# Performance work log

Measured on AMD Instinct MI355X. Metric: run time of the kernel, lower is better.

The kernel has to match this reference:

```python
import jax, jax.numpy as jnp
import numpy as np

EPS = 1e-5

def inorm(x):
    # instance norm over time (last) axis; torch.std is unbiased (ddof=1)
    m = jnp.mean(x, axis=-1, keepdims=True)
    s = jnp.sqrt(jnp.var(x, axis=-1, ddof=1, keepdims=True))
    return (x - m) / (s + EPS)

def tinorm(x):
    # time-wise instance norm: normalize over channel axis (dim=1)
    m = jnp.mean(x, axis=1, keepdims=True)
    s = jnp.sqrt(jnp.var(x, axis=1, ddof=1, keepdims=True))
    return (x - m) / (s + EPS)

def adaptive_norm(src, trg, wq, wk, wv, norm_fn):
    # src, trg: [B,C,T]; wq/wk/wv: [out,in] as in nn.Linear
    temp = src.shape[1] ** 0.5
    q = jnp.einsum('bct,oc->bto', norm_fn(src), wq)        # [B,Ts,C]
    k = jnp.einsum('bct,oc->bto', norm_fn(trg), wk)        # [B,Tt,C]
    v = jnp.einsum('bct,oc->bto', trg, wv)                 # [B,Tt,C]
    attn = jax.nn.softmax(jnp.einsum('bsc,btc->bst', q / temp, k), axis=-1)
    mean = jnp.einsum('bst,btc->bsc', attn, v)             # attn-weighted mean
    var = jax.nn.relu(jnp.einsum('bst,btc->bsc', attn, v * v) - mean * mean)
    mean_c = jnp.mean(mean, axis=1)[:, :, None]            # [B,C,1]
    std_c = jnp.sqrt(jnp.mean(var, axis=1))[:, :, None]    # [B,C,1]
    return std_c * inorm(src) + mean_c

def sap(x, w, b):
    # self-attention pooling over axis 1; x: [B,N,C], w: [C], b: [1]
    a = jax.nn.softmax(jnp.einsum('bnc,c->bn', x, w) + b, axis=-1)
    return jnp.einsum('bnc,bn->bc', x, a)

def setup_inputs():
    key = jax.random.key(0)
    ks = jax.random.split(key, 24)
    B, C, Ts, Tt, S = 4, 512, 2048, 2048, 2048
    sc = 1.0 / np.sqrt(C).astype(np.float32)
    return {
        'src': jax.random.normal(ks[0], (B, C, Ts), jnp.float32),
        'trg': jax.random.normal(ks[1], (B, C, Tt), jnp.float32),
        'means': jax.random.normal(ks[2], (B, S, C), jnp.float32),
        'stds': jax.random.uniform(ks[3], (B, S, C), jnp.float32),
        'wq_t': jax.random.normal(ks[4], (C, C), jnp.float32) * sc,
        'wk_t': jax.random.normal(ks[5], (C, C), jnp.float32) * sc,
        'wv_t': jax.random.normal(ks[6], (C, C), jnp.float32) * sc,
        'wq_c': jax.random.normal(ks[7], (C, C), jnp.float32) * sc,
        'wk_c': jax.random.normal(ks[8], (C, C), jnp.float32) * sc,
        'wv_c': jax.random.normal(ks[9], (C, C), jnp.float32) * sc,
        'conv1_w': jax.random.normal(ks[10], (C, 2 * C), jnp.float32) * sc,
        'conv1_b': jax.random.normal(ks[11], (C,), jnp.float32) * 0.02,
        'conv2_w': jax.random.normal(ks[12], (C, C, 3), jnp.float32) * sc,
        'bn_g': jax.random.uniform(ks[13], (C,), jnp.float32, 0.5, 1.5),
        'bn_b': jax.random.normal(ks[14], (C,), jnp.float32) * 0.05,
        'bn_m': jax.random.normal(ks[15], (C,), jnp.float32) * 0.1,
        'bn_v': jax.random.uniform(ks[16], (C,), jnp.float32, 0.5, 1.5),
        'msap_w': jax.random.normal(ks[17], (C,), jnp.float32) * sc,
        'msap_b': jax.random.normal(ks[18], (1,), jnp.float32) * 0.02,
        'ssap_w': jax.random.normal(ks[19], (C,), jnp.float32) * sc,
        'ssap_b': jax.random.normal(ks[20], (1,), jnp.float32) * 0.02,
    }

def reference(src, trg, means, stds, wq_t, wk_t, wv_t, wq_c, wk_c, wv_c,
              conv1_w, conv1_b, conv2_w, bn_g, bn_b, bn_m, bn_v,
              msap_w, msap_b, ssap_w, ssap_b):
    src1 = adaptive_norm(src, trg, wq_t, wk_t, wv_t, tinorm)   # TAN
    src2 = adaptive_norm(src, trg, wq_c, wk_c, wv_c, inorm)    # CAN
    x = jnp.concatenate([src1, src2], axis=1)                  # [B,2C,T]
    # conv1: kernel_size=1 -> pointwise GEMM
    x = jnp.einsum('bct,oc->bot', x, conv1_w) + conv1_b[None, :, None]
    # conv2: Conv1d(k=3, pad=1, bias=False) + BatchNorm1d(eval) + ReLU
    x = jax.lax.conv_general_dilated(x, conv2_w, (1,), 'SAME',
                                     dimension_numbers=('NCH', 'OIH', 'NCH'))
    x = (x - bn_m[None, :, None]) * jax.lax.rsqrt(bn_v[None, :, None] + EPS)
    x = x * bn_g[None, :, None] + bn_b[None, :, None]
    x = jax.nn.relu(x)
    # GLAN
    mean = sap(means, msap_w, msap_b)[:, :, None]              # [B,C,1]
    std = sap(stds, ssap_w, ssap_b)[:, :, None]                # [B,C,1]
    return inorm(x) * std + mean
```

## Files before the change

### kernel.cpp

```cpp
#include <hip/hip_runtime.h>
#include <cstdint>
#include <cstddef>

#define B_ 4
#define C_ 512
#define T_ 2048
#define S_ 2048
#define EPSF 1e-5f

typedef __bf16 bf16;
typedef __attribute__((ext_vector_type(8))) __bf16 bf16x8;
typedef __attribute__((ext_vector_type(4))) float f32x4;

__device__ __forceinline__ bf16 f2b(float f){ return (bf16)f; }
__device__ __forceinline__ float b2f(bf16 h){ return (float)h; }

__device__ __forceinline__ void gl_lds16(const void* g, void* l){
  __builtin_amdgcn_global_load_lds((__attribute__((address_space(1))) void*)(g),
                                   (__attribute__((address_space(3))) void*)(l), 16, 0, 0);
}

__device__ __forceinline__ float wave_sum(float v){
#pragma unroll
  for (int o = 32; o; o >>= 1) v += __shfl_xor(v, o, 64);
  return v;
}
__device__ __forceinline__ float wave_max(float v){
#pragma unroll
  for (int o = 32; o; o >>= 1) v = fmaxf(v, __shfl_xor(v, o, 64));
  return v;
}

template<int EPI, int TNW>
__global__ void __launch_bounds__(256) gemm_nt(
    const bf16* __restrict__ A, const bf16* __restrict__ Bm, void* __restrict__ Cout,
    int K, int lda, int ldb, int ldc,
    long long sA, long long sB, long long sC, long long sCb,
    int zdivA, int zmodB, float scale,
    const float* __restrict__ rs, const float* __restrict__ rsh,
    const float* __restrict__ cbias,
    float* __restrict__ osum, float* __restrict__ osum2, long long sRs)
{
  constexpr int TN = TNW*32;
  __shared__ alignas(16) bf16 lA[128*64];
  __shared__ alignas(16) bf16 lB[TN*64];
  const int tid = threadIdx.x;
  const int z = blockIdx.z;
  const bf16* Ab = A + (long long)(z / zdivA) * sA;
  const bf16* Bb = Bm + (long long)(z % zmodB) * sB;
  const int m0 = blockIdx.y*128, n0 = blockIdx.x*TN;
  const int lane = tid & 63, wvi = tid >> 6;
  const int wm = wvi >> 1, wn = wvi & 1;

  f32x4 acc[4][TNW] = {};

  const int lrow = tid >> 3;
  const int lcol = ((tid ^ lrow) & 7) * 8;
  const bf16* pa = Ab + (long long)(m0 + lrow)*lda + lcol;
  const bf16* pb = Bb + (long long)(n0 + lrow)*ldb + lcol;
  char* sa = (char*)lA + tid*16;
  char* sb = (char*)lB + tid*16;

  for (int k0 = 0; k0 < K; k0 += 64) {
#pragma unroll
    for (int it = 0; it < 4; ++it)
      gl_lds16(pa + (long long)it*32*lda + k0, sa + it*4096);
#pragma unroll
    for (int it = 0; it < TNW; ++it)
      gl_lds16(pb + (long long)it*32*ldb + k0, sb + it*4096);
    __syncthreads();
#pragma unroll
    for (int ks = 0; ks < 2; ++ks) {
      const int kq = ks*4 + (lane >> 4);
      bf16x8 af[4], bfr[TNW];
#pragma unroll
      for (int mt = 0; mt < 4; ++mt) {
        int r = wm*64 + mt*16 + (lane & 15);
        af[mt] = *(const bf16x8*)&lA[r*64 + ((kq ^ (r & 7))*8)];
      }
#pragma unroll
      for (int nt = 0; nt < TNW; ++nt) {
        int r = wn*(TNW*16) + nt*16 + (lane & 15);
        bfr[nt] = *(const bf16x8*)&lB[r*64 + ((kq ^ (r & 7))*8)];
      }
#pragma unroll
      for (int mt = 0; mt < 4; ++mt)
#pragma unroll
        for (int nt = 0; nt < TNW; ++nt)
          acc[mt][nt] = __builtin_amdgcn_mfma_f32_16x16x32_bf16(af[mt], bfr[nt], acc[mt][nt], 0, 0, 0);
    }
    __syncthreads();
  }

  if (EPI == 3) {
    float* red1 = (float*)lA;
    float* red2 = red1 + 4*TNW*16;
    const int cr = (lane >> 4)*4;
    float linv[4][4];
#pragma unroll
    for (int mt = 0; mt < 4; ++mt)
#pragma unroll
      for (int i = 0; i < 4; ++i)
        linv[mt][i] = 1.f / rs[(long long)z*sRs + (m0 + wm*64 + mt*16 + cr + i)];
    float s1[TNW], s2[TNW];
#pragma unroll
    for (int nt = 0; nt < TNW; ++nt) {
      s1[nt] = 0.f; s2[nt] = 0.f;
#pragma unroll
      for (int mt = 0; mt < 4; ++mt)
#pragma unroll
        for (int i = 0; i < 4; ++i) {
          float v = acc[mt][nt][i] * linv[mt][i];
          s1[nt] += v; s2[nt] += v*v;
        }
      s1[nt] += __shfl_xor(s1[nt], 16, 64);
      s1[nt] += __shfl_xor(s1[nt], 32, 64);
      s2[nt] += __shfl_xor(s2[nt], 16, 64);
      s2[nt] += __shfl_xor(s2[nt], 32, 64);
    }
    if (lane < 16) {
#pragma unroll
      for (int nt = 0; nt < TNW; ++nt) {
        red1[(wvi*TNW + nt)*16 + lane] = s1[nt];
        red2[(wvi*TNW + nt)*16 + lane] = s2[nt];
      }
    }
    __syncthreads();
    if (tid < 2*TN) {
      const int which = tid >= TN;
      const int col = tid - which*TN;
      const int wn2 = col / (TNW*16), rem = col % (TNW*16);
      const float* rr = which ? red2 : red1;
      float v = rr[wn2*(TNW*16) + rem] + rr[(2+wn2)*(TNW*16) + rem];
      float* dst = which ? osum2 : osum;
      atomicAdd(&dst[sCb*z + n0 + col], v);
    }
    return;
  }

  const int cr = (lane >> 4)*4, cc = lane & 15;
#pragma unroll
  for (int mt = 0; mt < 4; ++mt) {
#pragma unroll
    for (int i = 0; i < 4; ++i) {
      const int mm = m0 + wm*64 + mt*16 + cr + i;
      float rsum = 0.f, rsum2 = 0.f;
#pragma unroll
      for (int nt = 0; nt < TNW; ++nt) {
        const int nn = n0 + wn*(TNW*16) + nt*16 + cc;
        float v = acc[mt][nt][i];
        const long long co = sC*z + (long long)mm*ldc + nn;
        if (EPI == 0) {
          v *= scale;
          if (cbias) v += cbias[sCb*z + nn];
          ((bf16*)Cout)[co] = f2b(v);
        } else if (EPI == 2) {
          v = fmaxf(v*rs[mm] + rsh[mm], 0.f);
          ((float*)Cout)[co] = v;
          rsum += v; rsum2 += v*v;
        } else if (EPI == 4) {
          v = __expf(v);
          ((bf16*)Cout)[co] = f2b(v);
          rsum += v;
        }
      }
      if (EPI == 2 || EPI == 4) {
        rsum += __shfl_xor(rsum, 1, 64); rsum += __shfl_xor(rsum, 2, 64);
        rsum += __shfl_xor(rsum, 4, 64); rsum += __shfl_xor(rsum, 8, 64);
        if (EPI == 2) {
          rsum2 += __shfl_xor(rsum2, 1, 64); rsum2 += __shfl_xor(rsum2, 2, 64);
          rsum2 += __shfl_xor(rsum2, 4, 64); rsum2 += __shfl_xor(rsum2, 8, 64);
        }
        if (cc == 0) {
          atomicAdd(&osum[(long long)z*sRs + mm], rsum);
          if (EPI == 2) atomicAdd(&osum2[(long long)z*sRs + mm], rsum2);
        }
      }
    }
  }
}

__global__ void __launch_bounds__(256) row_stats_k(const float* __restrict__ X1,
    const float* __restrict__ X2, float* __restrict__ Mo, float* __restrict__ So, int n1)
{
  __shared__ float r1[4], r2[4];
  const int row = blockIdx.x;
  const float* x = (row < n1) ? X1 + (long long)row*T_ : X2 + (long long)(row-n1)*T_;
  float s1 = 0.f, s2 = 0.f;
  for (int i = threadIdx.x; i < T_; i += 256){ float v = x[i]; s1 += v; s2 += v*v; }
  s1 = wave_sum(s1); s2 = wave_sum(s2);
  const int lane = threadIdx.x & 63, w = threadIdx.x >> 6;
  if (!lane){ r1[w] = s1; r2[w] = s2; }
  __syncthreads();
  if (threadIdx.x == 0){
    s1 = r1[0]+r1[1]+r1[2]+r1[3];
    s2 = r2[0]+r2[1]+r2[2]+r2[3];
    float m = s1 * (1.f/T_);
    float var = (s2 - s1*m) * (1.f/(T_-1));
    Mo[row] = m; So[row] = sqrtf(fmaxf(var, 0.f));
  }
}

__global__ void __launch_bounds__(256) col_stats_k(const float* __restrict__ src,
    const float* __restrict__ trg, float* __restrict__ Mo, float* __restrict__ So)
{
  __shared__ float r1[4][64], r2[4][64];
  const int z = blockIdx.y, t0 = blockIdx.x*64;
  const float* X = (z < B_) ? src : trg;
  const int b = z & (B_-1);
  const int tl = threadIdx.x & 63, cg = threadIdx.x >> 6;
  float s1 = 0.f, s2 = 0.f;
  for (int c = cg; c < C_; c += 4) {
    float v = X[((long long)b*C_ + c)*T_ + t0 + tl];
    s1 += v; s2 += v*v;
  }
  r1[cg][tl] = s1; r2[cg][tl] = s2;
  __syncthreads();
  if (cg == 0) {
    s1 = r1[0][tl]+r1[1][tl]+r1[2][tl]+r1[3][tl];
    s2 = r2[0][tl]+r2[1][tl]+r2[2][tl]+r2[3][tl];
    float m = s1 * (1.f/C_);
    float var = (s2 - s1*m) * (1.f/(C_-1));
    Mo[z*T_ + t0 + tl] = m;
    So[z*T_ + t0 + tl] = sqrtf(fmaxf(var, 0.f));
  }
}

__global__ void __launch_bounds__(256) transform_k(const float* __restrict__ src,
    const float* __restrict__ trg,
    const float* __restrict__ tnm, const float* __restrict__ tns,
    const float* __restrict__ inm, const float* __restrict__ ins,
    bf16* __restrict__ NSt, bf16* __restrict__ NSc,
    bf16* __restrict__ NTt, bf16* __restrict__ NTc, bf16* __restrict__ TTr)
{
  __shared__ float tile[32][33];
  const int z = blockIdx.z, t0 = blockIdx.x*32, c0 = blockIdx.y*32;
  const int is_t = z >= B_, b = z & (B_-1);
  const float* X = is_t ? trg : src;
  const int tx = threadIdx.x, ty = threadIdx.y;
#pragma unroll
  for (int r = 0; r < 4; ++r) {
    int ci = ty + r*8;
    tile[ci][tx] = X[((long long)b*C_ + c0 + ci)*T_ + t0 + tx];
  }
  __syncthreads();
#pragma unroll
  for (int r = 0; r < 4; ++r) {
    int tj = ty + r*8, ci = tx;
    float v = tile[ci][tj];
    int gt = t0 + tj, gc = c0 + ci;
    float a = (v - tnm[z*T_ + gt]) / (tns[z*T_ + gt] + EPSF);
    float d = (v - inm[z*C_ + gc]) / (ins[z*C_ + gc] + EPSF);
    long long o = ((long long)b*T_ + gt)*C_ + gc;
    if (is_t) { NTt[o] = f2b(a); NTc[o] = f2b(d); TTr[o] = f2b(v); }
    else      { NSt[o] = f2b(a); NSc[o] = f2b(d); }
  }
}

__global__ void __launch_bounds__(256) softmax_row_k(const float* __restrict__ X, float* __restrict__ O)
{
  __shared__ float red[4];
  const long long row = blockIdx.x;
  const float* x = X + row*T_ + threadIdx.x*8;
  float v[8];
  f32x4 a0 = *(const f32x4*)x;
  f32x4 a1 = *(const f32x4*)(x + 4);
#pragma unroll
  for (int j = 0; j < 4; ++j){ v[j] = a0[j]; v[4+j] = a1[j]; }
  float m = -3.4e38f;
#pragma unroll
  for (int j = 0; j < 8; ++j) m = fmaxf(m, v[j]);
  m = wave_max(m);
  const int lane = threadIdx.x & 63, w = threadIdx.x >> 6;
  if (!lane) red[w] = m;
  __syncthreads();
  m = fmaxf(fmaxf(red[0], red[1]), fmaxf(red[2], red[3]));
  __syncthreads();
  float s = 0.f;
#pragma unroll
  for (int j = 0; j < 8; ++j){ v[j] = __expf(v[j] - m); s += v[j]; }
  s = wave_sum(s);
  if (!lane) red[w] = s;
  __syncthreads();
  s = red[0]+red[1]+red[2]+red[3];
  const float inv = 1.f/s;
  float* o = O + row*T_ + threadIdx.x*8;
#pragma unroll
  for (int j = 0; j < 8; ++j) o[j] = v[j]*inv;
}

__global__ void __launch_bounds__(256) colsum_k(const bf16* __restrict__ P,
    const float* __restrict__ l, float* __restrict__ cs)
{
  __shared__ float linv[256];
  const int t = blockIdx.x*256 + threadIdx.x;
  const int z = blockIdx.z;
  const long long s0 = (long long)blockIdx.y*256;
  linv[threadIdx.x] = 1.f / l[(long long)z*S_ + s0 + threadIdx.x];
  __syncthreads();
  const bf16* p = P + ((long long)z*S_ + s0)*T_ + t;
  float a = 0.f;
  for (int s = 0; s < 256; ++s) a += b2f(p[(long long)s*T_]) * linv[s];
  atomicAdd(&cs[z*T_ + t], a);
}

__global__ void __launch_bounds__(256) vv_fin_k(const float* __restrict__ cs,
    const bf16* __restrict__ VT, const float* __restrict__ msum,
    const float* __restrict__ m2sum, float* __restrict__ meanc, float* __restrict__ stdc)
{
  __shared__ float r1[4];
  const int c = blockIdx.x, z = blockIdx.y;
  const bf16* vr = VT + ((long long)z*C_ + c)*T_;
  const float* w = cs + z*T_;
  float a = 0.f;
  for (int t = threadIdx.x; t < T_; t += 256){ float v = b2f(vr[t]); a += w[t]*v*v; }
  a = wave_sum(a);
  const int lane = threadIdx.x & 63, wq = threadIdx.x >> 6;
  if (!lane) r1[wq] = a;
  __syncthreads();
  if (threadIdx.x == 0){
    a = r1[0]+r1[1]+r1[2]+r1[3];
    const int idx = z*C_ + c;
    meanc[idx] = msum[idx] * (1.f/S_);
    float var = (a - m2sum[idx]) * (1.f/S_);
    stdc[idx] = sqrtf(fmaxf(var, 0.f));
  }
}

__global__ void __launch_bounds__(256) weff_k(const float* __restrict__ w1,
    const float* __restrict__ b1, const float* __restrict__ sdt, const float* __restrict__ sdc,
    const float* __restrict__ mct, const float* __restrict__ mcc,
    bf16* __restrict__ Weff, float* __restrict__ beff)
{
  __shared__ float r1[4];
  const int o = blockIdx.x, b = blockIdx.y;
  float accb = 0.f;
  for (int c = threadIdx.x; c < C_; c += 256) {
    float wa = w1[o*2*C_ + c], wb = w1[o*2*C_ + C_ + c];
    Weff[((long long)(b*C_ + o))*C_ + c] = f2b(wa*sdt[b*C_+c] + wb*sdc[b*C_+c]);
    accb += wa*mct[b*C_+c] + wb*mcc[b*C_+c];
  }
  accb = wave_sum(accb);
  const int lane = threadIdx.x & 63, w = threadIdx.x >> 6;
  if (!lane) r1[w] = accb;
  __syncthreads();
  if (threadIdx.x == 0) beff[b*C_ + o] = b1[o] + r1[0]+r1[1]+r1[2]+r1[3];
}

__global__ void __launch_bounds__(256) w2r_k(const float* __restrict__ w2,
    const float* __restrict__ g, const float* __restrict__ be,
    const float* __restrict__ mu, const float* __restrict__ va,
    bf16* __restrict__ W2r, float* __restrict__ bnsc, float* __restrict__ bnsh)
{
  const int o = blockIdx.x;
  for (int c = threadIdx.x; c < C_; c += 256)
#pragma unroll
    for (int dt = 0; dt < 3; ++dt)
      W2r[(long long)o*3*C_ + dt*C_ + c] = f2b(w2[((long long)o*C_ + c)*3 + dt]);
  if (threadIdx.x == 0) {
    float s = g[o] * rsqrtf(va[o] + EPSF);
    bnsc[o] = s;
    bnsh[o] = be[o] - mu[o]*s;
  }
}

__global__ void __launch_bounds__(256) cast6_k(const float* __restrict__ a0,
    const float* __restrict__ a1, const float* __restrict__ a2, const float* __restrict__ a3,
    const float* __restrict__ a4, const float* __restrict__ a5, bf16* __restrict__ o)
{
  const int i = blockIdx.x*256 + threadIdx.x;
  const int slot = i >> 18;
  const float* srcs[6] = {a0,a1,a2,a3,a4,a5};
  const float sc = (slot < 2) ? 0.044194173824159216f : 1.f;
  o[i] = f2b(srcs[slot][i & 262143] * sc);
}

__global__ void __launch_bounds__(256) zero_pad_k(bf16* __restrict__ x1p)
{
  const int i = blockIdx.x*256 + threadIdx.x;
  const int b = i >> 10, rem = i & 1023;
  const long long row = (rem >> 9) ? (T_+1) : 0;
  const int c = rem & (C_-1);
  x1p[((long long)b*(T_+2) + row)*C_ + c] = f2b(0.f);
}

__global__ void __launch_bounds__(256) zero_f32_k(float* __restrict__ p)
{
  p[blockIdx.x*256 + threadIdx.x] = 0.f;
}

__global__ void __launch_bounds__(256) sap_logit_k(const float* __restrict__ means,
    const float* __restrict__ stds, const float* __restrict__ mw, const float* __restrict__ sw,
    const float* __restrict__ mb, const float* __restrict__ sb, float* __restrict__ out)
{
  const int n = blockIdx.x*4 + (threadIdx.x >> 6);
  const int z = blockIdx.y;
  const int sel = z >= B_, b = z & (B_-1);
  const float* x = sel ? stds : means;
  const float* w = sel ? sw : mw;
  const int lane = threadIdx.x & 63;
  const float* p = x + ((long long)b*S_ + n)*C_;
  float a = 0.f;
  for (int c = lane; c < C_; c += 64) a += p[c]*w[c];
  a = wave_sum(a);
  if (!lane) out[z*S_ + n] = a + (sel ? sb[0] : mb[0]);
}

__global__ void __launch_bounds__(256) sap_wsum_k(const float* __restrict__ means,
    const float* __restrict__ stds, const float* __restrict__ a, float* __restrict__ out)
{
  const int c = blockIdx.x*256 + threadIdx.x;
  const int z = blockIdx.z;
  const int sel = z >= B_, b = z & (B_-1);
  const float* x = sel ? stds : means;
  const long long n0 = (long long)blockIdx.y*256;
  const float* p = x + ((long long)b*S_ + n0)*C_ + c;
  const float* aw = a + z*S_ + n0;
  float acc = 0.f;
  for (int n = 0; n < 256; ++n) acc += p[(long long)n*C_] * aw[n];
  atomicAdd(&out[z*C_ + c], acc);
}

__global__ void __launch_bounds__(256) final_k(const float* __restrict__ y,
    const float* __restrict__ ysum, const float* __restrict__ y2sum,
    const float* __restrict__ sapms, float* __restrict__ out)
{
  const long long i = (long long)(blockIdx.x*256 + threadIdx.x) * 4;
  const long long r = i >> 11;
  const float s1 = ysum[r], s2 = y2sum[r];
  const float m = s1 * (1.f/T_);
  const float var = (s2 - s1*m) * (1.f/(T_-1));
  const float inv = 1.f/(sqrtf(fmaxf(var, 0.f)) + EPSF);
  const float mn = sapms[r], sd = sapms[B_*C_ + r];
  const f32x4 v = *(const f32x4*)(y + i);
  f32x4 o;
#pragma unroll
  for (int j = 0; j < 4; ++j) o[j] = (v[j] - m)*inv*sd + mn;
  *(f32x4*)(out + i) = o;
}

extern "C" void kernel_launch(void* const* d_in, const int* in_sizes, int n_in,
                              void* d_out, int out_size, void* d_ws, size_t ws_size,
                              hipStream_t stream)
{
  (void)in_sizes; (void)n_in; (void)out_size; (void)ws_size;
  const float* src    = (const float*)d_in[0];
  const float* trg    = (const float*)d_in[1];
  const float* means  = (const float*)d_in[2];
  const float* stds   = (const float*)d_in[3];
  const float* conv1w = (const float*)d_in[10];
  const float* conv1b = (const float*)d_in[11];
  const float* conv2w = (const float*)d_in[12];
  const float* bn_g   = (const float*)d_in[13];
  const float* bn_b   = (const float*)d_in[14];
  const float* bn_m   = (const float*)d_in[15];
  const float* bn_v   = (const float*)d_in[16];
  const float* msap_w = (const float*)d_in[17];
  const float* msap_b = (const float*)d_in[18];
  const float* ssap_w = (const float*)d_in[19];
  const float* ssap_b = (const float*)d_in[20];

  const long long BTC = (long long)B_*T_*C_;

  char* p = (char*)d_ws;
  auto take = [&](size_t n)->char*{ char* r = p; p += (n + 255) & ~(size_t)255; return r; };

  bf16* NSc = (bf16*)take(BTC*2);
  bf16* P2  = (bf16*)take((size_t)2*B_*S_*T_*2);
  bf16* NSt = P2;
  bf16* NTc = P2 + BTC;
  bf16* NTt = P2 + 2*BTC;
  bf16* TTr = P2 + 3*BTC;
  bf16* QK4 = (bf16*)take((size_t)4*BTC*2);
  bf16* VT2 = (bf16*)take((size_t)2*BTC*2);
  bf16* WQb = (bf16*)take((size_t)6*C_*C_*2);
  bf16* Weff= (bf16*)take((size_t)B_*C_*C_*2);
  bf16* W2r = (bf16*)take((size_t)C_*3*C_*2);
  bf16* x1p = (bf16*)take((size_t)B_*(T_+2)*C_*2);
  float* y  = (float*)take((size_t)B_*C_*T_*4);
  float* colsum = (float*)take(2*B_*T_*4);
  float* msum   = (float*)take(2*B_*C_*4);
  float* m2sum  = (float*)take(2*B_*C_*4);
  float* sapms  = (float*)take(2*B_*C_*4);
  float* lrow   = (float*)take(2*B_*S_*4);
  float* ysum   = (float*)take(B_*C_*4);
  float* y2sum  = (float*)take(B_*C_*4);
  float* tnm = (float*)take(2*B_*T_*4);
  float* tns = (float*)take(2*B_*T_*4);
  float* inm = (float*)take(2*B_*C_*4);
  float* ins = (float*)take(2*B_*C_*4);
  float* meanc = (float*)take(2*B_*C_*4);
  float* stdc  = (float*)take(2*B_*C_*4);
  float* beff  = (float*)take(B_*C_*4);
  float* bnsc  = (float*)take(C_*4);
  float* bnsh  = (float*)take(C_*4);
  float* sapl  = (float*)take(2*B_*S_*4);
  float* sapa  = (float*)take(2*B_*S_*4);

  dim3 blk(256);

  cast6_k<<<6144, blk, 0, stream>>>((const float*)d_in[7], (const float*)d_in[4],
      (const float*)d_in[8], (const float*)d_in[5], (const float*)d_in[9],
      (const float*)d_in[6], WQb);
  w2r_k<<<C_, blk, 0, stream>>>(conv2w, bn_g, bn_b, bn_m, bn_v, W2r, bnsc, bnsh);
  row_stats_k<<<2*B_*C_, blk, 0, stream>>>(src, trg, inm, ins, B_*C_);
  col_stats_k<<<dim3(T_/64, 2*B_), blk, 0, stream>>>(src, trg, tnm, tns);
  transform_k<<<dim3(T_/32, C_/32, 2*B_), dim3(32,8), 0, stream>>>(src, trg,
      tnm, tns, inm, ins, NSt, NSc, NTt, NTc, TTr);
  zero_pad_k<<<16, blk, 0, stream>>>(x1p);
  zero_f32_k<<<192, blk, 0, stream>>>(colsum);

  gemm_nt<0,4><<<dim3(C_/128, (B_*T_)/128, 4), blk, 0, stream>>>(NSc, WQb, QK4,
      C_, C_, C_, C_, BTC, (long long)C_*C_, BTC, 0, 1, 8, 1.f,
      nullptr, nullptr, nullptr, nullptr, nullptr, 0);
  gemm_nt<0,2><<<dim3(T_/64, C_/128, 8), blk, 0, stream>>>(WQb + (size_t)4*C_*C_, TTr, VT2,
      C_, C_, C_, T_, (long long)C_*C_, (long long)T_*C_, (long long)C_*T_, 0, 4, 4, 1.f,
      nullptr, nullptr, nullptr, nullptr, nullptr, 0);
  gemm_nt<4,4><<<dim3(T_/128, T_/128, 8), blk, 0, stream>>>(QK4, QK4 + 2*BTC, P2,
      C_, C_, C_, T_, (long long)T_*C_, (long long)T_*C_, (long long)S_*T_, 0, 1, 8, 1.f,
      nullptr, nullptr, nullptr, lrow, nullptr, S_);
  colsum_k<<<dim3(T_/256, S_/256, 8), blk, 0, stream>>>(P2, lrow, colsum);
  gemm_nt<3,4><<<dim3(C_/128, S_/128, 8), blk, 0, stream>>>(P2, VT2, nullptr,
      T_, T_, T_, 0, (long long)S_*T_, (long long)C_*T_, 0, C_, 1, 8, 1.f,
      lrow, nullptr, nullptr, msum, m2sum, S_);
  vv_fin_k<<<dim3(C_, 2*B_), blk, 0, stream>>>(colsum, VT2, msum, m2sum, meanc, stdc);

  weff_k<<<dim3(C_, B_), blk, 0, stream>>>(conv1w, conv1b,
      stdc + B_*C_, stdc, meanc + B_*C_, meanc, Weff, beff);
  gemm_nt<0,2><<<dim3(C_/64, T_/128, B_), blk, 0, stream>>>(NSc, Weff, x1p + C_,
      C_, C_, C_, C_, (long long)T_*C_, (long long)C_*C_, (long long)(T_+2)*C_, C_,
      1, 8, 1.f, nullptr, nullptr, beff, nullptr, nullptr, 0);
  gemm_nt<2,2><<<dim3(T_/64, C_/128, B_), blk, 0, stream>>>(W2r, x1p, y,
      3*C_, 3*C_, C_, T_, 0, (long long)(T_+2)*C_, (long long)C_*T_, 0,
      1, 8, 1.f, bnsc, bnsh, nullptr, ysum, y2sum, C_);

  sap_logit_k<<<dim3(S_/4, 2*B_), blk, 0, stream>>>(means, stds, msap_w, ssap_w,
      msap_b, ssap_b, sapl);
  softmax_row_k<<<2*B_, blk, 0, stream>>>(sapl, sapa);
  sap_wsum_k<<<dim3(C_/256, S_/256, 2*B_), blk, 0, stream>>>(means, stds, sapa, sapms);

  final_k<<<4096, blk, 0, stream>>>(y, ysum, y2sum, sapms, (float*)d_out);
}
```

Before: 453.4 us.

## Fuse stats passes, merge prep kernels, compute softmax row sums via MFMA

The separate row and column statistics kernels become one pass that produces per-time sums directly and per-channel sums through wave reductions and atomics. The normalization transform now derives mean and std from those raw sums. The softmax denominator is no longer reduced with atomics in the exp GEMM epilogue: the P·V GEMM computes it with an extra MFMA against a ones vector, from the bf16-rounded probabilities, and the P·V blocks are remapped in a 1D grid. Four small setup kernels (weight casts, conv weight reorder, padding zeroing, buffer zeroing) are merged into one launch to cut launch overhead, which relies on the accumulators being laid out contiguously.

```diff
diff --git a/kernel.cpp b/kernel.cpp
--- a/kernel.cpp
+++ b/kernel.cpp
@@ -44,15 +44,28 @@
   constexpr int TN = TNW*32;
   __shared__ alignas(16) bf16 lA[128*64];
   __shared__ alignas(16) bf16 lB[TN*64];
+  __shared__ float l_sh[128];
   const int tid = threadIdx.x;
-  const int z = blockIdx.z;
+  int z, m0, n0;
+  if (EPI == 3) {
+    const int id = blockIdx.x;
+    z = id & 7;
+    const int r = id >> 3;
+    n0 = (r & 3) * TN;
+    m0 = (r >> 2) * 128;
+  } else {
+    z = blockIdx.z; m0 = blockIdx.y*128; n0 = blockIdx.x*TN;
+  }
   const bf16* Ab = A + (long long)(z / zdivA) * sA;
   const bf16* Bb = Bm + (long long)(z % zmodB) * sB;
-  const int m0 = blockIdx.y*128, n0 = blockIdx.x*TN;
   const int lane = tid & 63, wvi = tid >> 6;
   const int wm = wvi >> 1, wn = wvi & 1;
 
   f32x4 acc[4][TNW] = {};
+  f32x4 accL[4] = {};
+  bf16x8 vone;
+#pragma unroll
+  for (int j = 0; j < 8; ++j) vone[j] = f2b(1.f);
 
   const int lrow = tid >> 3;
   const int lcol = ((tid ^ lrow) & 7) * 8;
@@ -88,20 +101,34 @@
 #pragma unroll
         for (int nt = 0; nt < TNW; ++nt)
           acc[mt][nt] = __builtin_amdgcn_mfma_f32_16x16x32_bf16(af[mt], bfr[nt], acc[mt][nt], 0, 0, 0);
+      if (EPI == 3 && wn == 0) {
+#pragma unroll
+        for (int mt = 0; mt < 4; ++mt)
+          accL[mt] = __builtin_amdgcn_mfma_f32_16x16x32_bf16(af[mt], vone, accL[mt], 0, 0, 0);
+      }
     }
     __syncthreads();
   }
 
   if (EPI == 3) {
+    if (wn == 0 && (lane & 15) == 0) {
+#pragma unroll
+      for (int mt = 0; mt < 4; ++mt)
+#pragma unroll
+        for (int i = 0; i < 4; ++i)
+          l_sh[wm*64 + mt*16 + (lane >> 4)*4 + i] = accL[mt][i];
+    }
+    __syncthreads();
+    if (n0 == 0 && tid < 128)
+      ((float*)Cout)[(long long)z*sC + m0 + tid] = l_sh[tid];
+    float linv[4][4];
+#pragma unroll
+    for (int mt = 0; mt < 4; ++mt)
+#pragma unroll
+      for (int i = 0; i < 4; ++i)
+        linv[mt][i] = 1.f / l_sh[wm*64 + mt*16 + (lane >> 4)*4 + i];
     float* red1 = (float*)lA;
     float* red2 = red1 + 4*TNW*16;
-    const int cr = (lane >> 4)*4;
-    float linv[4][4];
-#pragma unroll
-    for (int mt = 0; mt < 4; ++mt)
-#pragma unroll
-      for (int i = 0; i < 4; ++i)
-        linv[mt][i] = 1.f / rs[(long long)z*sRs + (m0 + wm*64 + mt*16 + cr + i)];
     float s1[TNW], s2[TNW];
 #pragma unroll
     for (int nt = 0; nt < TNW; ++nt) {
@@ -158,51 +185,27 @@
           v = fmaxf(v*rs[mm] + rsh[mm], 0.f);
           ((float*)Cout)[co] = v;
           rsum += v; rsum2 += v*v;
-        } else if (EPI == 4) {
-          v = __expf(v);
-          ((bf16*)Cout)[co] = f2b(v);
-          rsum += v;
+        } else if (EPI == 5) {
+          ((bf16*)Cout)[co] = f2b(__expf(v));
         }
       }
-      if (EPI == 2 || EPI == 4) {
+      if (EPI == 2) {
         rsum += __shfl_xor(rsum, 1, 64); rsum += __shfl_xor(rsum, 2, 64);
         rsum += __shfl_xor(rsum, 4, 64); rsum += __shfl_xor(rsum, 8, 64);
-        if (EPI == 2) {
-          rsum2 += __shfl_xor(rsum2, 1, 64); rsum2 += __shfl_xor(rsum2, 2, 64);
-          rsum2 += __shfl_xor(rsum2, 4, 64); rsum2 += __shfl_xor(rsum2, 8, 64);
-        }
+        rsum2 += __shfl_xor(rsum2, 1, 64); rsum2 += __shfl_xor(rsum2, 2, 64);
+        rsum2 += __shfl_xor(rsum2, 4, 64); rsum2 += __shfl_xor(rsum2, 8, 64);
         if (cc == 0) {
           atomicAdd(&osum[(long long)z*sRs + mm], rsum);
-          if (EPI == 2) atomicAdd(&osum2[(long long)z*sRs + mm], rsum2);
+          atomicAdd(&osum2[(long long)z*sRs + mm], rsum2);
         }
       }
     }
   }
 }
 
-__global__ void __launch_bounds__(256) row_stats_k(const float* __restrict__ X1,
-    const float* __restrict__ X2, float* __restrict__ Mo, float* __restrict__ So, int n1)
-{
-  __shared__ float r1[4], r2[4];
-  const int row = blockIdx.x;
-  const float* x = (row < n1) ? X1 + (long long)row*T_ : X2 + (long long)(row-n1)*T_;
-  float s1 = 0.f, s2 = 0.f;
-  for (int i = threadIdx.x; i < T_; i += 256){ float v = x[i]; s1 += v; s2 += v*v; }
-  s1 = wave_sum(s1); s2 = wave_sum(s2);
-  const int lane = threadIdx.x & 63, w = threadIdx.x >> 6;
-  if (!lane){ r1[w] = s1; r2[w] = s2; }
-  __syncthreads();
-  if (threadIdx.x == 0){
-    s1 = r1[0]+r1[1]+r1[2]+r1[3];
-    s2 = r2[0]+r2[1]+r2[2]+r2[3];
-    float m = s1 * (1.f/T_);
-    float var = (s2 - s1*m) * (1.f/(T_-1));
-    Mo[row] = m; So[row] = sqrtf(fmaxf(var, 0.f));
-  }
-}
-
-__global__ void __launch_bounds__(256) col_stats_k(const float* __restrict__ src,
-    const float* __restrict__ trg, float* __restrict__ Mo, float* __restrict__ So)
+__global__ void __launch_bounds__(256) stats_k(const float* __restrict__ src,
+    const float* __restrict__ trg, float* __restrict__ tsum, float* __restrict__ tsum2,
+    float* __restrict__ rsum, float* __restrict__ rsum2)
 {
   __shared__ float r1[4][64], r2[4][64];
   const int z = blockIdx.y, t0 = blockIdx.x*64;
@@ -213,23 +216,27 @@
   for (int c = cg; c < C_; c += 4) {
     float v = X[((long long)b*C_ + c)*T_ + t0 + tl];
     s1 += v; s2 += v*v;
+    float a  = wave_sum(v);
+    float a2 = wave_sum(v*v);
+    if (tl == 0) {
+      atomicAdd(&rsum[z*C_ + c], a);
+      atomicAdd(&rsum2[z*C_ + c], a2);
+    }
   }
   r1[cg][tl] = s1; r2[cg][tl] = s2;
   __syncthreads();
   if (cg == 0) {
     s1 = r1[0][tl]+r1[1][tl]+r1[2][tl]+r1[3][tl];
     s2 = r2[0][tl]+r2[1][tl]+r2[2][tl]+r2[3][tl];
-    float m = s1 * (1.f/C_);
-    float var = (s2 - s1*m) * (1.f/(C_-1));
-    Mo[z*T_ + t0 + tl] = m;
-    So[z*T_ + t0 + tl] = sqrtf(fmaxf(var, 0.f));
+    tsum[z*T_ + t0 + tl] = s1;
+    tsum2[z*T_ + t0 + tl] = s2;
   }
 }
 
 __global__ void __launch_bounds__(256) transform_k(const float* __restrict__ src,
     const float* __restrict__ trg,
-    const float* __restrict__ tnm, const float* __restrict__ tns,
-    const float* __restrict__ inm, const float* __restrict__ ins,
+    const float* __restrict__ tsum, const float* __restrict__ tsum2,
+    const float* __restrict__ rsum, const float* __restrict__ rsum2,
     bf16* __restrict__ NSt, bf16* __restrict__ NSc,
     bf16* __restrict__ NTt, bf16* __restrict__ NTc, bf16* __restrict__ TTr)
 {
@@ -249,8 +256,14 @@
     int tj = ty + r*8, ci = tx;
     float v = tile[ci][tj];
     int gt = t0 + tj, gc = c0 + ci;
-    float a = (v - tnm[z*T_ + gt]) / (tns[z*T_ + gt] + EPSF);
-    float d = (v - inm[z*C_ + gc]) / (ins[z*C_ + gc] + EPSF);
+    float ts1 = tsum[z*T_ + gt], ts2 = tsum2[z*T_ + gt];
+    float tm = ts1 * (1.f/C_);
+    float tsd = sqrtf(fmaxf((ts2 - ts1*tm) * (1.f/(C_-1)), 0.f)) + EPSF;
+    float rs1 = rsum[z*C_ + gc], rs2 = rsum2[z*C_ + gc];
+    float im = rs1 * (1.f/T_);
+    float isd = sqrtf(fmaxf((rs2 - rs1*im) * (1.f/(T_-1)), 0.f)) + EPSF;
+    float a = (v - tm) / tsd;
+    float d = (v - im) / isd;
     long long o = ((long long)b*T_ + gt)*C_ + gc;
     if (is_t) { NTt[o] = f2b(a); NTc[o] = f2b(d); TTr[o] = f2b(v); }
     else      { NSt[o] = f2b(a); NSc[o] = f2b(d); }
@@ -347,46 +360,44 @@
   if (threadIdx.x == 0) beff[b*C_ + o] = b1[o] + r1[0]+r1[1]+r1[2]+r1[3];
 }
 
-__global__ void __launch_bounds__(256) w2r_k(const float* __restrict__ w2,
-    const float* __restrict__ g, const float* __restrict__ be,
-    const float* __restrict__ mu, const float* __restrict__ va,
-    bf16* __restrict__ W2r, float* __restrict__ bnsc, float* __restrict__ bnsh)
-{
-  const int o = blockIdx.x;
-  for (int c = threadIdx.x; c < C_; c += 256)
-#pragma unroll
-    for (int dt = 0; dt < 3; ++dt)
-      W2r[(long long)o*3*C_ + dt*C_ + c] = f2b(w2[((long long)o*C_ + c)*3 + dt]);
-  if (threadIdx.x == 0) {
-    float s = g[o] * rsqrtf(va[o] + EPSF);
-    bnsc[o] = s;
-    bnsh[o] = be[o] - mu[o]*s;
-  }
-}
-
-__global__ void __launch_bounds__(256) cast6_k(const float* __restrict__ a0,
-    const float* __restrict__ a1, const float* __restrict__ a2, const float* __restrict__ a3,
-    const float* __restrict__ a4, const float* __restrict__ a5, bf16* __restrict__ o)
-{
-  const int i = blockIdx.x*256 + threadIdx.x;
-  const int slot = i >> 18;
-  const float* srcs[6] = {a0,a1,a2,a3,a4,a5};
-  const float sc = (slot < 2) ? 0.044194173824159216f : 1.f;
-  o[i] = f2b(srcs[slot][i & 262143] * sc);
-}
-
-__global__ void __launch_bounds__(256) zero_pad_k(bf16* __restrict__ x1p)
-{
-  const int i = blockIdx.x*256 + threadIdx.x;
-  const int b = i >> 10, rem = i & 1023;
-  const long long row = (rem >> 9) ? (T_+1) : 0;
-  const int c = rem & (C_-1);
-  x1p[((long long)b*(T_+2) + row)*C_ + c] = f2b(0.f);
-}
-
-__global__ void __launch_bounds__(256) zero_f32_k(float* __restrict__ p)
-{
-  p[blockIdx.x*256 + threadIdx.x] = 0.f;
+__global__ void __launch_bounds__(256) prep_k(
+    const float* __restrict__ a0, const float* __restrict__ a1,
+    const float* __restrict__ a2, const float* __restrict__ a3,
+    const float* __restrict__ a4, const float* __restrict__ a5,
+    bf16* __restrict__ WQb,
+    const float* __restrict__ w2, const float* __restrict__ g,
+    const float* __restrict__ be, const float* __restrict__ mu,
+    const float* __restrict__ va, bf16* __restrict__ W2r,
+    float* __restrict__ bnsc, float* __restrict__ bnsh,
+    bf16* __restrict__ x1p, float* __restrict__ zbase)
+{
+  const int bid = blockIdx.x, tid = threadIdx.x;
+  if (bid < 6144) {
+    const int i = bid*256 + tid;
+    const int slot = i >> 18;
+    const float* srcs[6] = {a0,a1,a2,a3,a4,a5};
+    const float sc = (slot < 2) ? 0.044194173824159216f : 1.f;
+    WQb[i] = f2b(srcs[slot][i & 262143] * sc);
+  } else if (bid < 6656) {
+    const int o = bid - 6144;
+    for (int c = tid; c < C_; c += 256)
+#pragma unroll
+      for (int dt = 0; dt < 3; ++dt)
+        W2r[(long long)o*3*C_ + dt*C_ + c] = f2b(w2[((long long)o*C_ + c)*3 + dt]);
+    if (tid == 0) {
+      float s = g[o] * rsqrtf(va[o] + EPSF);
+      bnsc[o] = s;
+      bnsh[o] = be[o] - mu[o]*s;
+    }
+  } else if (bid < 6672) {
+    const int i = (bid - 6656)*256 + tid;
+    const int b = i >> 10, rem = i & 1023;
+    const long long row = (rem >> 9) ? (T_+1) : 0;
+    const int c = rem & (C_-1);
+    x1p[((long long)b*(T_+2) + row)*C_ + c] = f2b(0.f);
+  } else {
+    zbase[(bid - 6672)*256 + tid] = 0.f;
+  }
 }
 
 __global__ void __launch_bounds__(256) sap_logit_k(const float* __restrict__ means,
@@ -485,10 +496,10 @@
   float* lrow   = (float*)take(2*B_*S_*4);
   float* ysum   = (float*)take(B_*C_*4);
   float* y2sum  = (float*)take(B_*C_*4);
-  float* tnm = (float*)take(2*B_*T_*4);
-  float* tns = (float*)take(2*B_*T_*4);
-  float* inm = (float*)take(2*B_*C_*4);
-  float* ins = (float*)take(2*B_*C_*4);
+  float* rsum   = (float*)take(2*B_*C_*4);
+  float* rsum2  = (float*)take(2*B_*C_*4);
+  float* tsum  = (float*)take(2*B_*T_*4);
+  float* tsum2 = (float*)take(2*B_*T_*4);
   float* meanc = (float*)take(2*B_*C_*4);
   float* stdc  = (float*)take(2*B_*C_*4);
   float* beff  = (float*)take(B_*C_*4);
@@ -499,16 +510,13 @@
 
   dim3 blk(256);
 
-  cast6_k<<<6144, blk, 0, stream>>>((const float*)d_in[7], (const float*)d_in[4],
+  prep_k<<<6896, blk, 0, stream>>>((const float*)d_in[7], (const float*)d_in[4],
       (const float*)d_in[8], (const float*)d_in[5], (const float*)d_in[9],
-      (const float*)d_in[6], WQb);
-  w2r_k<<<C_, blk, 0, stream>>>(conv2w, bn_g, bn_b, bn_m, bn_v, W2r, bnsc, bnsh);
-  row_stats_k<<<2*B_*C_, blk, 0, stream>>>(src, trg, inm, ins, B_*C_);
-  col_stats_k<<<dim3(T_/64, 2*B_), blk, 0, stream>>>(src, trg, tnm, tns);
+      (const float*)d_in[6], WQb, conv2w, bn_g, bn_b, bn_m, bn_v, W2r, bnsc, bnsh,
+      x1p, colsum);
+  stats_k<<<dim3(T_/64, 2*B_), blk, 0, stream>>>(src, trg, tsum, tsum2, rsum, rsum2);
   transform_k<<<dim3(T_/32, C_/32, 2*B_), dim3(32,8), 0, stream>>>(src, trg,
-      tnm, tns, inm, ins, NSt, NSc, NTt, NTc, TTr);
-  zero_pad_k<<<16, blk, 0, stream>>>(x1p);
-  zero_f32_k<<<192, blk, 0, stream>>>(colsum);
+      tsum, tsum2, rsum, rsum2, NSt, NSc, NTt, NTc, TTr);
 
   gemm_nt<0,4><<<dim3(C_/128, (B_*T_)/128, 4), blk, 0, stream>>>(NSc, WQb, QK4,
       C_, C_, C_, C_, BTC, (long long)C_*C_, BTC, 0, 1, 8, 1.f,
@@ -516,13 +524,13 @@
   gemm_nt<0,2><<<dim3(T_/64, C_/128, 8), blk, 0, stream>>>(WQb + (size_t)4*C_*C_, TTr, VT2,
       C_, C_, C_, T_, (long long)C_*C_, (long long)T_*C_, (long long)C_*T_, 0, 4, 4, 1.f,
       nullptr, nullptr, nullptr, nullptr, nullptr, 0);
-  gemm_nt<4,4><<<dim3(T_/128, T_/128, 8), blk, 0, stream>>>(QK4, QK4 + 2*BTC, P2,
+  gemm_nt<5,4><<<dim3(T_/128, T_/128, 8), blk, 0, stream>>>(QK4, QK4 + 2*BTC, P2,
       C_, C_, C_, T_, (long long)T_*C_, (long long)T_*C_, (long long)S_*T_, 0, 1, 8, 1.f,
-      nullptr, nullptr, nullptr, lrow, nullptr, S_);
+      nullptr, nullptr, nullptr, nullptr, nullptr, 0);
+  gemm_nt<3,4><<<dim3(512, 1, 1), blk, 0, stream>>>(P2, VT2, lrow,
+      T_, T_, T_, 0, (long long)S_*T_, (long long)C_*T_, S_, C_, 1, 8, 1.f,
+      nullptr, nullptr, nullptr, msum, m2sum, 0);
   colsum_k<<<dim3(T_/256, S_/256, 8), blk, 0, stream>>>(P2, lrow, colsum);
-  gemm_nt<3,4><<<dim3(C_/128, S_/128, 8), blk, 0, stream>>>(P2, VT2, nullptr,
-      T_, T_, T_, 0, (long long)S_*T_, (long long)C_*T_, 0, C_, 1, 8, 1.f,
-      lrow, nullptr, nullptr, msum, m2sum, S_);
   vv_fin_k<<<dim3(C_, 2*B_), blk, 0, stream>>>(colsum, VT2, msum, m2sum, meanc, stdc);
 
   weff_k<<<dim3(C_, B_), blk, 0, stream>>>(conv1w, conv1b,
```

Measured after the change: 509.2 us. 1.12x slower.
